# Kernel tuning notes

Hardware: AMD Instinct MI355X
Metric: run time of the kernel (lower is better)

Reference implementation:

```python
import jax, jax.numpy as jnp
import numpy as np

N = 50000      # nodes
E = 800000     # edges (avg degree 16)
IN = 128       # in_channels
OUT = 64       # out_channels
K = 2          # propagation hops


def setup_inputs() -> dict:
    key = jax.random.key(0)
    k1, k2, k3 = jax.random.split(key, 3)
    x = jax.random.normal(k1, (N, IN), dtype=jnp.float32)
    edge_index = jax.random.randint(k2, (2, E), 0, N, dtype=jnp.int32)
    # SGConv's internal Linear(in, out): weight [OUT, IN], bias [OUT]
    W = jax.random.normal(k3, (OUT, IN), dtype=jnp.float32) / np.sqrt(IN)
    b = jnp.zeros((OUT,), dtype=jnp.float32)
    return {"x": x, "edge_index": edge_index, "W": W, "b": b}


def reference(x, edge_index, W, b):
    # GCN normalization with self-loops (PyG gcn_norm, add_self_loops=True)
    row, col = edge_index[0], edge_index[1]
    loops = jnp.arange(N, dtype=edge_index.dtype)
    row = jnp.concatenate([row, loops])   # source nodes
    col = jnp.concatenate([col, loops])   # target nodes
    ones = jnp.ones((E + N,), dtype=x.dtype)
    deg = jax.ops.segment_sum(ones, col, num_segments=N)          # in-degree incl. self-loop
    deg_inv_sqrt = jnp.where(deg > 0, jax.lax.rsqrt(deg), 0.0)
    norm = deg_inv_sqrt[row] * deg_inv_sqrt[col]                  # [E+N]

    # K-hop propagation: x <- D^{-1/2} (A+I) D^{-1/2} x
    for _ in range(K):
        x = jax.ops.segment_sum(x[row] * norm[:, None], col, num_segments=N)

    # final linear; dropout is identity in eval mode (training=False)
    return x @ W.T + b
```

## Files before the change

kernel.cpp:

```cpp
#include <hip/hip_runtime.h>
#include <hip/hip_bf16.h>
#include <hip/hip_fp16.h>

#define IN_CH 128
#define OUT_CH 64
#define NB 512

__global__ void __launch_bounds__(512) histo_kernel(const int* __restrict__ col,
                                                    int* __restrict__ blkcnt,
                                                    int E, int chunk) {
    __shared__ int h[256];
    int blk = blockIdx.x, tid = threadIdx.x;
    if (tid < 256) h[tid] = 0;
    __syncthreads();
    int s = blk * chunk, e = min(s + chunk, E);
    for (int i = s + tid; i < e; i += 512)
        atomicAdd(&h[col[i] >> 8], 1);
    __syncthreads();
    if (tid < 256) blkcnt[blk * 256 + tid] = h[tid];
}

__global__ void __launch_bounds__(256) scanblk_kernel(int* __restrict__ blkcnt,
                                                      int* __restrict__ totals) {
    __shared__ int ps[256];
    int b = blockIdx.x, tid = threadIdx.x;
    int i0 = (2 * tid) * 256 + b, i1 = (2 * tid + 1) * 256 + b;
    int a0 = blkcnt[i0], a1 = blkcnt[i1];
    int lsum = a0 + a1;
    ps[tid] = lsum;
    __syncthreads();
    for (int d = 1; d < 256; d <<= 1) {
        int t = 0;
        if (tid >= d) t = ps[tid - d];
        __syncthreads();
        if (tid >= d) ps[tid] += t;
        __syncthreads();
    }
    int excl = ps[tid] - lsum;
    blkcnt[i0] = excl;
    blkcnt[i1] = excl + a0;
    if (tid == 255) totals[b] = excl + lsum;
}

__global__ void __launch_bounds__(512) bucket_scatter_kernel(const int* __restrict__ row,
                                                             const int* __restrict__ col,
                                                             const int* __restrict__ blkcnt,
                                                             const int* __restrict__ totals,
                                                             unsigned int* __restrict__ tmp,
                                                             int E, int chunk, int nbkt) {
    __shared__ int ps[256];
    __shared__ int cur[256];
    int blk = blockIdx.x, tid = threadIdx.x;
    int v = 0;
    if (tid < 256) { v = (tid < nbkt) ? totals[tid] : 0; ps[tid] = v; }
    __syncthreads();
    for (int d = 1; d < 256; d <<= 1) {
        int t = 0;
        if (tid < 256 && tid >= d) t = ps[tid - d];
        __syncthreads();
        if (tid < 256 && tid >= d) ps[tid] += t;
        __syncthreads();
    }
    if (tid < 256) cur[tid] = (ps[tid] - v) + blkcnt[blk * 256 + tid];
    __syncthreads();
    int s = blk * chunk, e = min(s + chunk, E);
    for (int i = s + tid; i < e; i += 512) {
        int c = col[i], r = row[i];
        int p = atomicAdd(&cur[c >> 8], 1);
        tmp[p] = ((unsigned)(c & 255) << 16) | (unsigned)r;
    }
}

__global__ void __launch_bounds__(512) bucket_sort_kernel(const unsigned int* __restrict__ tmp,
                                                          const int* __restrict__ totals,
                                                          int* __restrict__ off,
                                                          float* __restrict__ dis,
                                                          unsigned short* __restrict__ eidx,
                                                          int nbkt, int E, int n) {
    __shared__ int bs[256];
    __shared__ int cntl[256];
    __shared__ int sc[256];
    __shared__ int posl[256];
    int b = blockIdx.x, tid = threadIdx.x;
    int v = 0;
    if (tid < 256) { v = (tid < nbkt) ? totals[tid] : 0; bs[tid] = v; }
    __syncthreads();
    for (int d = 1; d < 256; d <<= 1) {
        int t = 0;
        if (tid < 256 && tid >= d) t = bs[tid - d];
        __syncthreads();
        if (tid < 256 && tid >= d) bs[tid] += t;
        __syncthreads();
    }
    if (tid < 256) bs[tid] -= v;
    if (tid < 256) cntl[tid] = 0;
    __syncthreads();
    int s = bs[b];
    int e = s + ((b < nbkt) ? totals[b] : 0);
    for (int i = s + tid; i < e; i += 512)
        atomicAdd(&cntl[tmp[i] >> 16], 1);
    __syncthreads();
    int c = 0, excl = 0;
    if (tid < 256) { c = cntl[tid]; sc[tid] = c; }
    __syncthreads();
    for (int d = 1; d < 256; d <<= 1) {
        int t = 0;
        if (tid < 256 && tid >= d) t = sc[tid - d];
        __syncthreads();
        if (tid < 256 && tid >= d) sc[tid] += t;
        __syncthreads();
    }
    if (tid < 256) {
        excl = sc[tid] - c;
        int gid = (b << 8) + tid;
        if (gid < n) {
            off[gid] = s + excl;
            dis[gid] = rsqrtf((float)(c + 1));
        }
        posl[tid] = s + excl;
    }
    if (b == 0 && tid == 0) off[n] = E;
    __syncthreads();
    for (int i = s + tid; i < e; i += 512) {
        unsigned int w = tmp[i];
        int p = atomicAdd(&posl[w >> 16], 1);
        eidx[p] = (unsigned short)(w & 0xFFFFu);
    }
}

__global__ void __launch_bounds__(256, 2) gemm_kernel(const float* __restrict__ x,
                                                      const float* __restrict__ W,
                                                      const float* __restrict__ dis,
                                                      __half* __restrict__ z, int n) {
    __shared__ float Xs[64 * 132];
    __shared__ float Ws[64 * 132];
    int t = threadIdx.x;
    int m0 = blockIdx.x * 64;
#pragma unroll
    for (int r = 0; r < 8; ++r) {
        int f = t + 256 * r;
        int o = f >> 5, kq = f & 31;
        float4 w = ((const float4*)W)[f];
        *(float4*)&Ws[o * 132 + kq * 4] = w;
    }
#pragma unroll
    for (int r = 0; r < 8; ++r) {
        int f = t + 256 * r;
        int node = f >> 5, kq = f & 31;
        int gv = min(m0 + node, n - 1);
        float4 xv = ((const float4*)(x + (size_t)gv * IN_CH))[kq];
        *(float4*)&Xs[node * 132 + kq * 4] = xv;
    }
    __syncthreads();
    int tx = t & 15, ty = t >> 4;
    float acc[4][4];
#pragma unroll
    for (int i = 0; i < 4; ++i)
#pragma unroll
        for (int j = 0; j < 4; ++j) acc[i][j] = 0.f;

#pragma unroll 4
    for (int kq = 0; kq < 32; ++kq) {
        float4 xa[4], wb[4];
#pragma unroll
        for (int i = 0; i < 4; ++i) xa[i] = *(const float4*)&Xs[(tx + 16 * i) * 132 + kq * 4];
#pragma unroll
        for (int j = 0; j < 4; ++j) wb[j] = *(const float4*)&Ws[(ty * 4 + j) * 132 + kq * 4];
#pragma unroll
        for (int i = 0; i < 4; ++i)
#pragma unroll
            for (int j = 0; j < 4; ++j) {
                float s = acc[i][j];
                s = fmaf(xa[i].x, wb[j].x, s);
                s = fmaf(xa[i].y, wb[j].y, s);
                s = fmaf(xa[i].z, wb[j].z, s);
                s = fmaf(xa[i].w, wb[j].w, s);
                acc[i][j] = s;
            }
    }
#pragma unroll
    for (int i = 0; i < 4; ++i) {
        int v = m0 + tx + 16 * i;
        if (v < n) {
            float dv = dis[v];
            union { __half2 h[2]; float2 f; } u;
            u.h[0] = __floats2half2_rn(dv * acc[i][0], dv * acc[i][1]);
            u.h[1] = __floats2half2_rn(dv * acc[i][2], dv * acc[i][3]);
            *(float2*)&z[(size_t)v * OUT_CH + ty * 4] = u.f;
        }
    }
}

template <int MODE>
__global__ void __launch_bounds__(256) hop_kernel(const __half* __restrict__ zin,
                                                  void* __restrict__ out,
                                                  const unsigned short* __restrict__ eidx,
                                                  const int* __restrict__ off,
                                                  const float* __restrict__ dis,
                                                  const float* __restrict__ bias, int n) {
    int v = (int)((blockIdx.x * 256 + threadIdx.x) >> 6);
    if (v >= n) return;
    int lane = threadIdx.x & 63;
    int grp = lane >> 3;
    int sub = lane & 7;
    int s = off[v], e = off[v + 1];
    float a0 = 0.f, a1 = 0.f, a2 = 0.f, a3 = 0.f;
    float a4 = 0.f, a5 = 0.f, a6 = 0.f, a7 = 0.f;
    if (grp == 0) {
        float4 raw = ((const float4*)(zin + (size_t)v * OUT_CH))[sub];
        const __half2* h2 = (const __half2*)&raw;
        float2 f0 = __half22float2(h2[0]), f1 = __half22float2(h2[1]);
        float2 f2 = __half22float2(h2[2]), f3 = __half22float2(h2[3]);
        a0 = f0.x; a1 = f0.y; a2 = f1.x; a3 = f1.y;
        a4 = f2.x; a5 = f2.y; a6 = f3.x; a7 = f3.y;
    }
    int i = s + grp;
    bool have = (i < e);
    int r = have ? (int)eidx[i] : 0;
    while (have) {
        int j = i + 8;
        bool hnext = (j < e);
        int rn = hnext ? (int)eidx[j] : 0;
        float4 raw = ((const float4*)(zin + (size_t)r * OUT_CH))[sub];
        const __half2* h2 = (const __half2*)&raw;
        float2 f0 = __half22float2(h2[0]), f1 = __half22float2(h2[1]);
        float2 f2 = __half22float2(h2[2]), f3 = __half22float2(h2[3]);
        a0 += f0.x; a1 += f0.y; a2 += f1.x; a3 += f1.y;
        a4 += f2.x; a5 += f2.y; a6 += f3.x; a7 += f3.y;
        r = rn; i = j; have = hnext;
    }
#pragma unroll
    for (int m = 8; m <= 32; m <<= 1) {
        a0 += __shfl_xor(a0, m, 64); a1 += __shfl_xor(a1, m, 64);
        a2 += __shfl_xor(a2, m, 64); a3 += __shfl_xor(a3, m, 64);
        a4 += __shfl_xor(a4, m, 64); a5 += __shfl_xor(a5, m, 64);
        a6 += __shfl_xor(a6, m, 64); a7 += __shfl_xor(a7, m, 64);
    }
    if (grp == 0) {
        float dv = dis[v];
        if (MODE == 0) {
            float sc = dv * dv;
            union { __half2 h[4]; float4 f; } u;
            u.h[0] = __floats2half2_rn(sc * a0, sc * a1);
            u.h[1] = __floats2half2_rn(sc * a2, sc * a3);
            u.h[2] = __floats2half2_rn(sc * a4, sc * a5);
            u.h[3] = __floats2half2_rn(sc * a6, sc * a7);
            ((float4*)((__half*)out + (size_t)v * OUT_CH))[sub] = u.f;
        } else {
            const float4* bp = (const float4*)(bias + sub * 8);
            float4 b0 = bp[0], b1 = bp[1];
            float* op = (float*)out + (size_t)v * OUT_CH + sub * 8;
            *(float4*)op = make_float4(fmaf(dv, a0, b0.x), fmaf(dv, a1, b0.y),
                                       fmaf(dv, a2, b0.z), fmaf(dv, a3, b0.w));
            *(float4*)(op + 4) = make_float4(fmaf(dv, a4, b1.x), fmaf(dv, a5, b1.y),
                                             fmaf(dv, a6, b1.z), fmaf(dv, a7, b1.w));
        }
    }
}

extern "C" void kernel_launch(void* const* d_in, const int* in_sizes, int n_in,
                              void* d_out, int out_size, void* d_ws, size_t ws_size,
                              hipStream_t stream) {
    const float* x = (const float*)d_in[0];
    const int* ei = (const int*)d_in[1];
    const float* W = (const float*)d_in[2];
    const float* b = (const float*)d_in[3];
    int n = in_sizes[0] / IN_CH;
    int E = in_sizes[1] / 2;
    const int* row = ei;
    const int* col = ei + E;

    char* ws = (char*)d_ws;
    size_t o = 0;
    auto alloc = [&](size_t bytes) -> void* {
        void* p = ws + o;
        o += (bytes + 255) & ~(size_t)255;
        return p;
    };
    int nbkt = (n + 255) >> 8;
    int chunk = (E + NB - 1) / NB;

    int*            blkcnt = (int*)alloc((size_t)NB * 256 * 4);
    int*            totals = (int*)alloc(256 * 4);
    unsigned int*   tmp    = (unsigned int*)alloc((size_t)E * 4);
    int*            off    = (int*)alloc((size_t)(n + 1) * 4);
    float*          dis    = (float*)alloc((size_t)n * 4);
    unsigned short* eidx   = (unsigned short*)alloc((size_t)E * 2);
    __half*         zA     = (__half*)alloc((size_t)n * OUT_CH * 2);
    __half*         zB     = (__half*)alloc((size_t)n * OUT_CH * 2);

    histo_kernel<<<NB, 512, 0, stream>>>(col, blkcnt, E, chunk);
    scanblk_kernel<<<nbkt, 256, 0, stream>>>(blkcnt, totals);
    bucket_scatter_kernel<<<NB, 512, 0, stream>>>(row, col, blkcnt, totals, tmp, E, chunk, nbkt);
    bucket_sort_kernel<<<nbkt, 512, 0, stream>>>(tmp, totals, off, dis, eidx, nbkt, E, n);
    gemm_kernel<<<(n + 63) / 64, 256, 0, stream>>>(x, W, dis, zA, n);
    int hopBlocks = (n + 3) / 4;
    hop_kernel<0><<<hopBlocks, 256, 0, stream>>>(zA, zB, eidx, off, dis, nullptr, n);
    hop_kernel<1><<<hopBlocks, 256, 0, stream>>>(zB, d_out, eidx, off, dis, b, n);
}
```

Measured before the change: 167.9 us.

## Split each hop into two source-half passes to keep gathered rows cache-resident

```diff
diff --git a/kernel.cpp b/kernel.cpp
--- a/kernel.cpp
+++ b/kernel.cpp
@@ -5,6 +5,8 @@
 #define IN_CH 128
 #define OUT_CH 64
 #define NB 512
+
+typedef float nf4 __attribute__((ext_vector_type(4)));
 
 __global__ void __launch_bounds__(512) histo_kernel(const int* __restrict__ col,
                                                     int* __restrict__ blkcnt,
@@ -74,13 +76,14 @@
 __global__ void __launch_bounds__(512) bucket_sort_kernel(const unsigned int* __restrict__ tmp,
                                                           const int* __restrict__ totals,
                                                           int* __restrict__ off,
+                                                          int* __restrict__ mid,
                                                           float* __restrict__ dis,
                                                           unsigned short* __restrict__ eidx,
-                                                          int nbkt, int E, int n) {
+                                                          int nbkt, int E, int n, int nhalf) {
     __shared__ int bs[256];
-    __shared__ int cntl[256];
-    __shared__ int sc[256];
-    __shared__ int posl[256];
+    __shared__ int cntl[512];
+    __shared__ int sc[512];
+    __shared__ int posl[512];
     int b = blockIdx.x, tid = threadIdx.x;
     int v = 0;
     if (tid < 256) { v = (tid < nbkt) ? totals[tid] : 0; bs[tid] = v; }
@@ -93,37 +96,43 @@
         __syncthreads();
     }
     if (tid < 256) bs[tid] -= v;
-    if (tid < 256) cntl[tid] = 0;
+    cntl[tid] = 0;
     __syncthreads();
     int s = bs[b];
     int e = s + ((b < nbkt) ? totals[b] : 0);
-    for (int i = s + tid; i < e; i += 512)
-        atomicAdd(&cntl[tmp[i] >> 16], 1);
-    __syncthreads();
-    int c = 0, excl = 0;
-    if (tid < 256) { c = cntl[tid]; sc[tid] = c; }
-    __syncthreads();
-    for (int d = 1; d < 256; d <<= 1) {
+    for (int i = s + tid; i < e; i += 512) {
+        unsigned int w = tmp[i];
+        int key = ((w >> 16) << 1) | (((int)(w & 0xFFFFu) >= nhalf) ? 1 : 0);
+        atomicAdd(&cntl[key], 1);
+    }
+    __syncthreads();
+    int c = cntl[tid];
+    sc[tid] = c;
+    __syncthreads();
+    for (int d = 1; d < 512; d <<= 1) {
         int t = 0;
-        if (tid < 256 && tid >= d) t = sc[tid - d];
-        __syncthreads();
-        if (tid < 256 && tid >= d) sc[tid] += t;
-        __syncthreads();
-    }
+        if (tid >= d) t = sc[tid - d];
+        __syncthreads();
+        if (tid >= d) sc[tid] += t;
+        __syncthreads();
+    }
+    posl[tid] = s + (sc[tid] - c);
+    __syncthreads();
     if (tid < 256) {
-        excl = sc[tid] - c;
         int gid = (b << 8) + tid;
         if (gid < n) {
-            off[gid] = s + excl;
-            dis[gid] = rsqrtf((float)(c + 1));
+            int cl = cntl[2 * tid], ch = cntl[2 * tid + 1];
+            off[gid] = s + (sc[2 * tid] - cl);
+            mid[gid] = s + (sc[2 * tid + 1] - ch);
+            dis[gid] = rsqrtf((float)(cl + ch + 1));
         }
-        posl[tid] = s + excl;
     }
     if (b == 0 && tid == 0) off[n] = E;
     __syncthreads();
     for (int i = s + tid; i < e; i += 512) {
         unsigned int w = tmp[i];
-        int p = atomicAdd(&posl[w >> 16], 1);
+        int key = ((w >> 16) << 1) | (((int)(w & 0xFFFFu) >= nhalf) ? 1 : 0);
+        int p = atomicAdd(&posl[key], 1);
         eidx[p] = (unsigned short)(w & 0xFFFFu);
     }
 }
@@ -191,22 +200,21 @@
     }
 }
 
-template <int MODE>
-__global__ void __launch_bounds__(256) hop_kernel(const __half* __restrict__ zin,
-                                                  void* __restrict__ out,
-                                                  const unsigned short* __restrict__ eidx,
-                                                  const int* __restrict__ off,
-                                                  const float* __restrict__ dis,
-                                                  const float* __restrict__ bias, int n) {
+__global__ void __launch_bounds__(256) hopA_kernel(const __half* __restrict__ zin,
+                                                   float* __restrict__ partial,
+                                                   const unsigned short* __restrict__ eidx,
+                                                   const int* __restrict__ off,
+                                                   const int* __restrict__ mid,
+                                                   int n, int nhalf) {
     int v = (int)((blockIdx.x * 256 + threadIdx.x) >> 6);
     if (v >= n) return;
     int lane = threadIdx.x & 63;
     int grp = lane >> 3;
     int sub = lane & 7;
-    int s = off[v], e = off[v + 1];
+    int s = off[v], m = mid[v];
     float a0 = 0.f, a1 = 0.f, a2 = 0.f, a3 = 0.f;
     float a4 = 0.f, a5 = 0.f, a6 = 0.f, a7 = 0.f;
-    if (grp == 0) {
+    if (grp == 0 && v < nhalf) {
         float4 raw = ((const float4*)(zin + (size_t)v * OUT_CH))[sub];
         const __half2* h2 = (const __half2*)&raw;
         float2 f0 = __half22float2(h2[0]), f1 = __half22float2(h2[1]);
@@ -215,6 +223,70 @@
         a4 = f2.x; a5 = f2.y; a6 = f3.x; a7 = f3.y;
     }
     int i = s + grp;
+    bool have = (i < m);
+    int r = have ? (int)eidx[i] : 0;
+    while (have) {
+        int j = i + 8;
+        bool hnext = (j < m);
+        int rn = hnext ? (int)eidx[j] : 0;
+        float4 raw = ((const float4*)(zin + (size_t)r * OUT_CH))[sub];
+        const __half2* h2 = (const __half2*)&raw;
+        float2 f0 = __half22float2(h2[0]), f1 = __half22float2(h2[1]);
+        float2 f2 = __half22float2(h2[2]), f3 = __half22float2(h2[3]);
+        a0 += f0.x; a1 += f0.y; a2 += f1.x; a3 += f1.y;
+        a4 += f2.x; a5 += f2.y; a6 += f3.x; a7 += f3.y;
+        r = rn; i = j; have = hnext;
+    }
+#pragma unroll
+    for (int mm = 8; mm <= 32; mm <<= 1) {
+        a0 += __shfl_xor(a0, mm, 64); a1 += __shfl_xor(a1, mm, 64);
+        a2 += __shfl_xor(a2, mm, 64); a3 += __shfl_xor(a3, mm, 64);
+        a4 += __shfl_xor(a4, mm, 64); a5 += __shfl_xor(a5, mm, 64);
+        a6 += __shfl_xor(a6, mm, 64); a7 += __shfl_xor(a7, mm, 64);
+    }
+    if (grp == 0) {
+        float* pp = partial + (size_t)v * OUT_CH + sub * 8;
+        nf4 s0 = {a0, a1, a2, a3};
+        nf4 s1 = {a4, a5, a6, a7};
+        __builtin_nontemporal_store(s0, (nf4*)pp);
+        __builtin_nontemporal_store(s1, (nf4*)(pp + 4));
+    }
+}
+
+template <int MODE>
+__global__ void __launch_bounds__(256) hopB_kernel(const __half* __restrict__ zin,
+                                                   const float* __restrict__ partial,
+                                                   void* __restrict__ out,
+                                                   const unsigned short* __restrict__ eidx,
+                                                   const int* __restrict__ off,
+                                                   const int* __restrict__ mid,
+                                                   const float* __restrict__ dis,
+                                                   const float* __restrict__ bias,
+                                                   int n, int nhalf) {
+    int v = (int)((blockIdx.x * 256 + threadIdx.x) >> 6);
+    if (v >= n) return;
+    int lane = threadIdx.x & 63;
+    int grp = lane >> 3;
+    int sub = lane & 7;
+    int m = mid[v], e = off[v + 1];
+    float a0 = 0.f, a1 = 0.f, a2 = 0.f, a3 = 0.f;
+    float a4 = 0.f, a5 = 0.f, a6 = 0.f, a7 = 0.f;
+    if (grp == 0) {
+        const float* pp = partial + (size_t)v * OUT_CH + sub * 8;
+        nf4 p0 = __builtin_nontemporal_load((const nf4*)pp);
+        nf4 p1 = __builtin_nontemporal_load((const nf4*)(pp + 4));
+        a0 = p0.x; a1 = p0.y; a2 = p0.z; a3 = p0.w;
+        a4 = p1.x; a5 = p1.y; a6 = p1.z; a7 = p1.w;
+        if (v >= nhalf) {
+            float4 raw = ((const float4*)(zin + (size_t)v * OUT_CH))[sub];
+            const __half2* h2 = (const __half2*)&raw;
+            float2 f0 = __half22float2(h2[0]), f1 = __half22float2(h2[1]);
+            float2 f2 = __half22float2(h2[2]), f3 = __half22float2(h2[3]);
+            a0 += f0.x; a1 += f0.y; a2 += f1.x; a3 += f1.y;
+            a4 += f2.x; a5 += f2.y; a6 += f3.x; a7 += f3.y;
+        }
+    }
+    int i = m + grp;
     bool have = (i < e);
     int r = have ? (int)eidx[i] : 0;
     while (have) {
@@ -230,11 +302,11 @@
         r = rn; i = j; have = hnext;
     }
 #pragma unroll
-    for (int m = 8; m <= 32; m <<= 1) {
-        a0 += __shfl_xor(a0, m, 64); a1 += __shfl_xor(a1, m, 64);
-        a2 += __shfl_xor(a2, m, 64); a3 += __shfl_xor(a3, m, 64);
-        a4 += __shfl_xor(a4, m, 64); a5 += __shfl_xor(a5, m, 64);
-        a6 += __shfl_xor(a6, m, 64); a7 += __shfl_xor(a7, m, 64);
+    for (int mm = 8; mm <= 32; mm <<= 1) {
+        a0 += __shfl_xor(a0, mm, 64); a1 += __shfl_xor(a1, mm, 64);
+        a2 += __shfl_xor(a2, mm, 64); a3 += __shfl_xor(a3, mm, 64);
+        a4 += __shfl_xor(a4, mm, 64); a5 += __shfl_xor(a5, mm, 64);
+        a6 += __shfl_xor(a6, mm, 64); a7 += __shfl_xor(a7, mm, 64);
     }
     if (grp == 0) {
         float dv = dis[v];
@@ -250,10 +322,12 @@
             const float4* bp = (const float4*)(bias + sub * 8);
             float4 b0 = bp[0], b1 = bp[1];
             float* op = (float*)out + (size_t)v * OUT_CH + sub * 8;
-            *(float4*)op = make_float4(fmaf(dv, a0, b0.x), fmaf(dv, a1, b0.y),
-                                       fmaf(dv, a2, b0.z), fmaf(dv, a3, b0.w));
-            *(float4*)(op + 4) = make_float4(fmaf(dv, a4, b1.x), fmaf(dv, a5, b1.y),
-                                             fmaf(dv, a6, b1.z), fmaf(dv, a7, b1.w));
+            nf4 s0 = {fmaf(dv, a0, b0.x), fmaf(dv, a1, b0.y),
+                      fmaf(dv, a2, b0.z), fmaf(dv, a3, b0.w)};
+            nf4 s1 = {fmaf(dv, a4, b1.x), fmaf(dv, a5, b1.y),
+                      fmaf(dv, a6, b1.z), fmaf(dv, a7, b1.w)};
+            __builtin_nontemporal_store(s0, (nf4*)op);
+            __builtin_nontemporal_store(s1, (nf4*)(op + 4));
         }
     }
 }
@@ -269,6 +343,7 @@
     int E = in_sizes[1] / 2;
     const int* row = ei;
     const int* col = ei + E;
+    int nhalf = n / 2;
 
     char* ws = (char*)d_ws;
     size_t o = 0;
@@ -284,17 +359,21 @@
     int*            totals = (int*)alloc(256 * 4);
     unsigned int*   tmp    = (unsigned int*)alloc((size_t)E * 4);
     int*            off    = (int*)alloc((size_t)(n + 1) * 4);
+    int*            midp   = (int*)alloc((size_t)n * 4);
     float*          dis    = (float*)alloc((size_t)n * 4);
     unsigned short* eidx   = (unsigned short*)alloc((size_t)E * 2);
     __half*         zA     = (__half*)alloc((size_t)n * OUT_CH * 2);
     __half*         zB     = (__half*)alloc((size_t)n * OUT_CH * 2);
+    float*          part   = (float*)alloc((size_t)n * OUT_CH * 4);
 
     histo_kernel<<<NB, 512, 0, stream>>>(col, blkcnt, E, chunk);
     scanblk_kernel<<<nbkt, 256, 0, stream>>>(blkcnt, totals);
     bucket_scatter_kernel<<<NB, 512, 0, stream>>>(row, col, blkcnt, totals, tmp, E, chunk, nbkt);
-    bucket_sort_kernel<<<nbkt, 512, 0, stream>>>(tmp, totals, off, dis, eidx, nbkt, E, n);
+    bucket_sort_kernel<<<nbkt, 512, 0, stream>>>(tmp, totals, off, midp, dis, eidx, nbkt, E, n, nhalf);
     gemm_kernel<<<(n + 63) / 64, 256, 0, stream>>>(x, W, dis, zA, n);
     int hopBlocks = (n + 3) / 4;
-    hop_kernel<0><<<hopBlocks, 256, 0, stream>>>(zA, zB, eidx, off, dis, nullptr, n);
-    hop_kernel<1><<<hopBlocks, 256, 0, stream>>>(zB, d_out, eidx, off, dis, b, n);
-}
+    hopA_kernel<<<hopBlocks, 256, 0, stream>>>(zA, part, eidx, off, midp, n, nhalf);
+    hopB_kernel<0><<<hopBlocks, 256, 0, stream>>>(zA, part, zB, eidx, off, midp, dis, nullptr, n, nhalf);
+    hopA_kernel<<<hopBlocks, 256, 0, stream>>>(zB, part, eidx, off, midp, n, nhalf);
+    hopB_kernel<1><<<hopBlocks, 256, 0, stream>>>(zB, part, d_out, eidx, off, midp, dis, b, n, nhalf);
+}
```

After: 198.0 us. 18.0% more time.
